# Kernel optimization log

Measured on AMD Instinct MI355X. Metric: run time of the kernel, lower is better.

## Reference

```python
import jax, jax.numpy as jnp
import numpy as np
import math

B, NB, NA, NC, D, E, H = 4, 2048, 1024, 1024, 1024, 8, 16
HD = D // H
TOP_K = 2
T_MAX = 1000.0
TAU_MIN, TAU_MAX = 0.5, 2.0
W_MIN, W_MAX = 0.1, 0.2
CAP_LO, CAP_HI = 0.5, 0.6
FLOOR = min(0.05, 0.15 / E)       # cfg.routing_floor property
ALPHA = min(FLOOR * E, 1.0)       # routing-floor interpolation weight
BIAS_COEFF = 0.01
EPS = 1e-8


def _layernorm(x, g, b, eps=1e-5):
    mu = x.mean(-1, keepdims=True)
    var = ((x - mu) ** 2).mean(-1, keepdims=True)
    return (x - mu) * jax.lax.rsqrt(var + eps) * g + b


def _forward(tokens_B, output_A, output_C, in_proj_w, in_proj_b, out_proj_w, out_proj_b,
             ln_g, ln_b, te_w1, te_b1, te_w2, te_b2,
             gate_w1, gate_b1, gate_w2, gate_b2, expert_bias, t):
    t_norm = t.astype(jnp.float32) / T_MAX                 # (B,)
    ctx_C = jax.lax.stop_gradient(output_C)                # stopgrad_C_to_B
    ctx_AC = jnp.concatenate([output_A, ctx_C], axis=1)    # (B, NA+NC, D)

    # --- cross attention (torch nn.MultiheadAttention, batch_first) ---
    wq, wk, wv = jnp.split(in_proj_w, 3, axis=0)
    bq, bk, bv = jnp.split(in_proj_b, 3)
    q = (tokens_B @ wq.T + bq).reshape(B, NB, H, HD)
    k = (ctx_AC @ wk.T + bk).reshape(B, NA + NC, H, HD)
    v = (ctx_AC @ wv.T + bv).reshape(B, NA + NC, H, HD)
    scores = jnp.einsum('bqhd,bkhd->bhqk', q, k) / math.sqrt(HD)
    attn = jax.nn.softmax(scores, axis=-1)
    ctx = jnp.einsum('bhqk,bkhd->bqhd', attn, v).reshape(B, NB, D)
    ctx_B = ctx @ out_proj_w.T + out_proj_b
    ctx_B = _layernorm(ctx_B + tokens_B, ln_g, ln_b)

    # --- sinusoidal timestep embedding + 2-layer MLP ---
    half = D // 2
    freq = jnp.exp(-math.log(10000.0) * jnp.arange(half, dtype=jnp.float32) / (half - 1))
    args = t.astype(jnp.float32)[:, None] * freq
    emb = jnp.concatenate([jnp.sin(args), jnp.cos(args)], axis=-1)   # (B, D)
    t_emb = jax.nn.silu(emb @ te_w1.T + te_b1) @ te_w2.T + te_b2     # (B, D)
    t_emb = jnp.broadcast_to(t_emb[:, None, :], (B, NB, D))

    # --- gate MLP + expert bias + temperature ---
    gate_in = jnp.concatenate([tokens_B, ctx_B, t_emb], axis=-1)     # (B, NB, 3D)
    logits = jax.nn.relu(gate_in @ gate_w1.T + gate_b1) @ gate_w2.T + gate_b2 + expert_bias
    tau = (TAU_MIN + (TAU_MAX - TAU_MIN) * t_norm)[:, None, None]
    probs = jax.nn.softmax(logits / tau, axis=-1)                    # (B, NB, E)

    # routing floor: interpolate toward uniform
    probs = (1.0 - ALPHA) * probs + ALPHA / E

    # shared expert injection: expert 0 gets scheduled weight w(t), rest renormalised
    w = (W_MIN + (W_MAX - W_MIN) * t_norm)[:, None, None]
    shared = jnp.maximum(probs[..., 0:1], w)
    others = probs[..., 1:]
    others = others / jnp.maximum(others.sum(-1, keepdims=True), EPS) * (1.0 - shared)
    probs = jnp.concatenate([shared, others], axis=-1)

    # top-k mask (keep top-k probs, zero the rest)
    vals, idx = jax.lax.top_k(probs, TOP_K)
    dispatch = (jax.nn.one_hot(idx, E, dtype=probs.dtype) * vals[..., None]).sum(-2)

    # token-level hard cap (torch.no_grad -> stop_gradient) with redistribution
    cap = (CAP_LO + (CAP_HI - CAP_LO) * t_norm)[:, None, None]
    excess = jax.nn.relu(dispatch - cap)
    capped = dispatch - excess
    headroom = jax.nn.relu(cap - capped)
    head_sum = jnp.maximum(headroom.sum(-1, keepdims=True), EPS)
    capped = capped + excess.sum(-1, keepdims=True) * (headroom / head_sum)
    dispatch = jax.lax.stop_gradient(capped)

    # batch-level utilisation penalty on specialists 1..E-1
    fair = NB / max(E - 1, 1)
    load = dispatch.sum(axis=1).mean(axis=0)                          # (E,)
    pen_excess = jax.nn.relu(load[1:] - fair * 1.5)
    bias_penalty = BIAS_COEFF * jnp.sum(pen_excess ** 2)

    combine = dispatch / (dispatch.sum(-1, keepdims=True) + EPS)
    return dispatch, combine, bias_penalty


def setup_inputs() -> dict:
    key = jax.random.key(0)
    ks = jax.random.split(key, 12)
    g = lambda k, sh: jax.random.normal(k, sh, jnp.float32) * 0.02
    return dict(
        tokens_B=jax.random.normal(ks[0], (B, NB, D), jnp.float32),
        output_A=jax.random.normal(ks[1], (B, NA, D), jnp.float32),
        output_C=jax.random.normal(ks[2], (B, NC, D), jnp.float32),
        t=jax.random.randint(ks[3], (B,), 0, 1000, jnp.int32),
        in_proj_w=g(ks[4], (3 * D, D)),
        in_proj_b=jnp.zeros((3 * D,), jnp.float32),
        out_proj_w=g(ks[5], (D, D)),
        out_proj_b=jnp.zeros((D,), jnp.float32),
        ln_g=jnp.ones((D,), jnp.float32),
        ln_b=jnp.zeros((D,), jnp.float32),
        te_w1=g(ks[6], (2 * D, D)),
        te_b1=jnp.zeros((2 * D,), jnp.float32),
        te_w2=g(ks[7], (D, 2 * D)),
        te_b2=jnp.zeros((D,), jnp.float32),
        gate_w1=g(ks[8], (D, 3 * D)),
        gate_b1=jnp.zeros((D,), jnp.float32),
        gate_w2=g(ks[9], (E, D)),
        gate_b2=jnp.zeros((E,), jnp.float32),
        expert_bias=jnp.zeros((E,), jnp.float32),
    )


def reference(tokens_B, output_A, output_C, t, in_proj_w, in_proj_b, out_proj_w, out_proj_b,
              ln_g, ln_b, te_w1, te_b1, te_w2, te_b2,
              gate_w1, gate_b1, gate_w2, gate_b2, expert_bias):
    return _forward(tokens_B, output_A, output_C, in_proj_w, in_proj_b, out_proj_w, out_proj_b,
                    ln_g, ln_b, te_w1, te_b1, te_w2, te_b2,
                    gate_w1, gate_b1, gate_w2, gate_b2, expert_bias, t)
```

## Files before the change

### kernel.cpp

```cpp
#include <hip/hip_runtime.h>
#include <math.h>


typedef __attribute__((ext_vector_type(8))) short short8;
typedef __attribute__((ext_vector_type(4))) float f32x4;
typedef unsigned short u16;
typedef unsigned int u32;

__global__ void zero_k(double* p) {
    if (threadIdx.x < 8) p[threadIdx.x] = 0.0;
}

__device__ inline u16 bf_hi(float x) {
    u32 u = __float_as_uint(x);
    u += 0x7FFFu + ((u >> 16) & 1u);
    return (u16)(u >> 16);
}
__device__ inline u16 bf_lo(float x, u16 h) {
    float hf = __uint_as_float(((u32)h) << 16);
    return bf_hi(x - hf);
}
__device__ inline u32 pack_bf(float x) {
    u32 u = __float_as_uint(x);
    u32 hi = (u + (0x7FFFu + ((u >> 16) & 1u))) >> 16;
    float hf = __uint_as_float(hi << 16);
    float d = x - hf;
    u32 u2 = __float_as_uint(d);
    u32 lo = (u2 + (0x7FFFu + ((u2 >> 16) & 1u))) >> 16;
    return (hi << 16) | lo;
}

__global__ __launch_bounds__(256)
void split_k(const float* __restrict__ in, u16* __restrict__ hi,
             u16* __restrict__ lo, int n4) {
    int i = blockIdx.x * 256 + threadIdx.x;
    if (i >= n4) return;
    float4 x = ((const float4*)in)[i];
    ushort4 h, l;
    h.x = bf_hi(x.x); l.x = bf_lo(x.x, h.x);
    h.y = bf_hi(x.y); l.y = bf_lo(x.y, h.y);
    h.z = bf_hi(x.z); l.z = bf_lo(x.z, h.z);
    h.w = bf_hi(x.w); l.w = bf_lo(x.w, h.w);
    ((ushort4*)hi)[i] = h;
    ((ushort4*)lo)[i] = l;
}

__global__ void emb_k(const int* __restrict__ t, float* __restrict__ emb) {
    int b = blockIdx.x;
    int j = threadIdx.x;
    float x1 = (float)(-9.210340371976184) * (float)j;
    float x2 = x1 / 511.0f;
    float freq = (float)exp((double)x2);
    float tf = (float)t[b];
    float arg = tf * freq;
    emb[b * 1024 + j]       = (float)sin((double)arg);
    emb[b * 1024 + 512 + j] = (float)cos((double)arg);
}

__global__ void te_fc_k(const float* __restrict__ in, const float* __restrict__ W,
                        const float* __restrict__ bias, float* __restrict__ out,
                        int K, int N, int do_silu) {
    int b = blockIdx.x;
    int wv = threadIdx.x >> 6, lane = threadIdx.x & 63;
    const float* inb = in + (size_t)b * K;
    int n0 = blockIdx.y * 16 + wv * 4;
    for (int q = 0; q < 4; q++) {
        int n = n0 + q;
        const float* wr = W + (size_t)n * K;
        float acc = 0.f;
        for (int c = lane * 4; c < K; c += 256) {
            float4 a  = *(const float4*)(inb + c);
            float4 w4 = *(const float4*)(wr + c);
            acc += a.x * w4.x + a.y * w4.y + a.z * w4.z + a.w * w4.w;
        }
#pragma unroll
        for (int off = 1; off < 64; off <<= 1) acc += __shfl_xor(acc, off, 64);
        if (lane == 0) {
            float x = acc + bias[n];
            out[(size_t)b * N + n] = do_silu ? (x / (1.0f + expf(-x))) : x;
        }
    }
}

template<bool GATE, bool RELU, int OMODE>
__global__ __launch_bounds__(256, 2)
void bfgemm_k(const u16* __restrict__ A0h, const u16* __restrict__ A0l,
              const u16* __restrict__ A1h, const u16* __restrict__ A1l,
              const u16* __restrict__ A2h, const u16* __restrict__ A2l,
              const u16* __restrict__ Wh_g, const u16* __restrict__ Wl_g,
              const float* __restrict__ bias, float* __restrict__ C,
              u16* __restrict__ Chi, u16* __restrict__ Clo, int K)
{
    __shared__ u16 Ah[128 * 32];
    __shared__ u16 Al[128 * 32];
    __shared__ u16 Wh[128 * 32];
    __shared__ u16 Wl[128 * 32];
    const int tid = threadIdx.x;
    const int row0 = blockIdx.x * 128;
    const int col0 = blockIdx.y * 128;
    const int wv = tid >> 6;
    const int lane = tid & 63;
    const int wrow = (wv & 1) * 64;
    const int wcol = (wv >> 1) * 64;
    const int l15 = lane & 15, quad = lane >> 4;

    f32x4 acc[4][4];
#pragma unroll
    for (int i = 0; i < 4; i++)
#pragma unroll
        for (int j = 0; j < 4; j++)
            acc[i][j] = (f32x4){0.f, 0.f, 0.f, 0.f};

    const int ar0 = tid >> 2, ak0 = (tid & 3) * 8;
    const int ar1 = (tid + 256) >> 2, ak1 = ((tid + 256) & 3) * 8;

    for (int kc = 0; kc < K; kc += 32) {
        const u16* pAh = A0h;
        const u16* pAl = A0l;
        int kk = kc;
        int tembseg = 0;
        if (GATE) {
            int seg = kc >> 10;
            if (seg == 1) { pAh = A1h; pAl = A1l; }
            else if (seg == 2) { pAh = A2h; pAl = A2l; tembseg = 1; }
            kk = kc & 1023;
        }
        const int astr = GATE ? 1024 : K;
        int g0 = row0 + ar0, g1 = row0 + ar1;
        if (GATE && tembseg) { g0 >>= 11; g1 >>= 11; }
        uint4 vah0 = *(const uint4*)&pAh[(size_t)g0 * astr + kk + ak0];
        uint4 vah1 = *(const uint4*)&pAh[(size_t)g1 * astr + kk + ak1];
        uint4 val0 = *(const uint4*)&pAl[(size_t)g0 * astr + kk + ak0];
        uint4 val1 = *(const uint4*)&pAl[(size_t)g1 * astr + kk + ak1];
        uint4 vwh0 = *(const uint4*)&Wh_g[(size_t)(col0 + ar0) * K + kc + ak0];
        uint4 vwh1 = *(const uint4*)&Wh_g[(size_t)(col0 + ar1) * K + kc + ak1];
        uint4 vwl0 = *(const uint4*)&Wl_g[(size_t)(col0 + ar0) * K + kc + ak0];
        uint4 vwl1 = *(const uint4*)&Wl_g[(size_t)(col0 + ar1) * K + kc + ak1];
        __syncthreads();
        *(uint4*)&Ah[ar0 * 32 + ak0] = vah0;
        *(uint4*)&Ah[ar1 * 32 + ak1] = vah1;
        *(uint4*)&Al[ar0 * 32 + ak0] = val0;
        *(uint4*)&Al[ar1 * 32 + ak1] = val1;
        *(uint4*)&Wh[ar0 * 32 + ak0] = vwh0;
        *(uint4*)&Wh[ar1 * 32 + ak1] = vwh1;
        *(uint4*)&Wl[ar0 * 32 + ak0] = vwl0;
        *(uint4*)&Wl[ar1 * 32 + ak1] = vwl1;
        __syncthreads();

        short8 a_h[4], a_l[4];
#pragma unroll
        for (int i = 0; i < 4; i++) {
            int r = (wrow + i * 16 + l15) * 32 + quad * 8;
            a_h[i] = *(const short8*)&Ah[r];
            a_l[i] = *(const short8*)&Al[r];
        }
#pragma unroll
        for (int j = 0; j < 4; j++) {
            int c = (wcol + j * 16 + l15) * 32 + quad * 8;
            short8 b_h = *(const short8*)&Wh[c];
            short8 b_l = *(const short8*)&Wl[c];
#pragma unroll
            for (int i = 0; i < 4; i++) {
                acc[i][j] = __builtin_amdgcn_mfma_f32_16x16x32_bf16(a_h[i], b_h, acc[i][j], 0, 0, 0);
                acc[i][j] = __builtin_amdgcn_mfma_f32_16x16x32_bf16(a_h[i], b_l, acc[i][j], 0, 0, 0);
                acc[i][j] = __builtin_amdgcn_mfma_f32_16x16x32_bf16(a_l[i], b_h, acc[i][j], 0, 0, 0);
            }
        }
    }

#pragma unroll
    for (int i = 0; i < 4; i++) {
#pragma unroll
        for (int j = 0; j < 4; j++) {
            int cc = col0 + wcol + j * 16 + l15;
#pragma unroll
            for (int r = 0; r < 4; r++) {
                int rr = row0 + wrow + i * 16 + quad * 4 + r;
                float v = acc[i][j][r] + ((OMODE == 3) ? bias[rr] : bias[cc]);
                if (RELU) v = fmaxf(v, 0.f);
                if (OMODE == 0) {
                    C[(size_t)rr * 1024 + cc] = v;
                } else if (OMODE == 1) {
                    u32 pk = pack_bf(v);
                    size_t a = (size_t)rr * 1024 + cc;
                    Chi[a] = (u16)(pk >> 16); Clo[a] = (u16)pk;
                } else if (OMODE == 2) {
                    int orow = ((rr >> 10) & 3) * 2048 + (rr >> 12) * 1024 + (rr & 1023);
                    u32 pk = pack_bf(v);
                    size_t a = (size_t)orow * 1024 + cc;
                    Chi[a] = (u16)(pk >> 16); Clo[a] = (u16)pk;
                } else {
                    int bb2 = (cc >> 10) & 3;
                    int key = (cc >> 12) * 1024 + (cc & 1023);
                    u32 pk = pack_bf(v);
                    size_t a = ((size_t)(bb2 * 1024 + rr)) * 2048 + key;
                    Chi[a] = (u16)(pk >> 16); Clo[a] = (u16)pk;
                }
            }
        }
    }
}

__global__ __launch_bounds__(512, 1)
void attn_k(const u16* Qh, const u16* Ql,
            const u16* __restrict__ Kh, const u16* __restrict__ Kl,
            const u16* __restrict__ Vh, const u16* __restrict__ Vl,
            u16* Oh, u16* Ol)
{
    __shared__ u32 Pu[256 * 76];
    __shared__ u16 Vsm[2][64 * 72];
    u16* Ksh = (u16*)Pu;
    u16* Ksl = Ksh + 64 * 72;

    const int tid = threadIdx.x;
    const int w = tid >> 6, lane = tid & 63;
    const int l15 = lane & 15, quad = lane >> 4;
    const int bh = blockIdx.x, b = bh >> 4, h = bh & 15;
    const int qw = blockIdx.y * 256 + w * 32;
    const int qrow0 = b * 2048 + qw;

    short8 qh_f[2][2], ql_f[2][2];
#pragma unroll
    for (int i = 0; i < 2; i++)
#pragma unroll
        for (int kc = 0; kc < 2; kc++) {
            size_t a = (size_t)(qrow0 + i * 16 + l15) * 1024 + h * 64 + kc * 32 + quad * 8;
            qh_f[i][kc] = *(const short8*)&Qh[a];
            ql_f[i][kc] = *(const short8*)&Ql[a];
        }

    const int skey = tid >> 3, sdb = (tid & 7) * 8;
    const int lds_k = skey * 72 + sdb;
    const size_t g_k = ((size_t)(b * 2048) + skey) * 1024 + h * 64 + sdb;
    const int vd = tid >> 3, vkb = (tid & 7) * 8;
    const int lds_v = vd * 72 + vkb;
    const size_t g_v = ((size_t)((b * 16 + h) * 64 + vd)) * 2048 + vkb;

    uint4 pk_h = *(const uint4*)&Kh[g_k];
    uint4 pk_l = *(const uint4*)&Kl[g_k];
    uint4 pv_h = *(const uint4*)&Vh[g_v];
    uint4 pv_l = *(const uint4*)&Vl[g_v];

    f32x4 o[2][4];
#pragma unroll
    for (int i = 0; i < 2; i++)
#pragma unroll
        for (int j = 0; j < 4; j++) o[i][j] = (f32x4){0.f, 0.f, 0.f, 0.f};
    float lsum[2][4] = {};

    for (int kt = 0; kt < 32; kt++) {
        __syncthreads();
        *(uint4*)&Ksh[lds_k] = pk_h;
        *(uint4*)&Ksl[lds_k] = pk_l;
        *(uint4*)&Vsm[0][lds_v] = pv_h;
        *(uint4*)&Vsm[1][lds_v] = pv_l;
        __syncthreads();
        if (kt < 31) {
            size_t gk2 = g_k + (size_t)(kt + 1) * 65536;
            size_t gv2 = g_v + (size_t)(kt + 1) * 64;
            pk_h = *(const uint4*)&Kh[gk2];
            pk_l = *(const uint4*)&Kl[gk2];
            pv_h = *(const uint4*)&Vh[gv2];
            pv_l = *(const uint4*)&Vl[gv2];
        }
        f32x4 s[2][4];
#pragma unroll
        for (int i = 0; i < 2; i++)
#pragma unroll
            for (int j = 0; j < 4; j++) s[i][j] = (f32x4){0.f, 0.f, 0.f, 0.f};
#pragma unroll
        for (int j = 0; j < 4; j++) {
            int ka = (j * 16 + l15) * 72 + quad * 8;
            short8 kh0 = *(const short8*)&Ksh[ka];
            short8 kh1 = *(const short8*)&Ksh[ka + 32];
            short8 kl0 = *(const short8*)&Ksl[ka];
            short8 kl1 = *(const short8*)&Ksl[ka + 32];
#pragma unroll
            for (int i = 0; i < 2; i++) {
                s[i][j] = __builtin_amdgcn_mfma_f32_16x16x32_bf16(qh_f[i][0], kh0, s[i][j], 0, 0, 0);
                s[i][j] = __builtin_amdgcn_mfma_f32_16x16x32_bf16(qh_f[i][0], kl0, s[i][j], 0, 0, 0);
                s[i][j] = __builtin_amdgcn_mfma_f32_16x16x32_bf16(ql_f[i][0], kh0, s[i][j], 0, 0, 0);
                s[i][j] = __builtin_amdgcn_mfma_f32_16x16x32_bf16(qh_f[i][1], kh1, s[i][j], 0, 0, 0);
                s[i][j] = __builtin_amdgcn_mfma_f32_16x16x32_bf16(qh_f[i][1], kl1, s[i][j], 0, 0, 0);
                s[i][j] = __builtin_amdgcn_mfma_f32_16x16x32_bf16(ql_f[i][1], kh1, s[i][j], 0, 0, 0);
            }
        }
        __syncthreads();
#pragma unroll
        for (int i = 0; i < 2; i++)
#pragma unroll
            for (int j = 0; j < 4; j++)
#pragma unroll
                for (int r = 0; r < 4; r++) {
                    float p = __expf(s[i][j][r] * 0.125f);
                    lsum[i][r] += p;
                    Pu[(w * 32 + i * 16 + quad * 4 + r) * 76 + j * 16 + l15] = pack_bf(p);
                }
#pragma unroll
        for (int kc = 0; kc < 2; kc++) {
            short8 ph[2], pl[2];
#pragma unroll
            for (int i = 0; i < 2; i++) {
                const uint4* pp = (const uint4*)&Pu[(w * 32 + i * 16 + l15) * 76 + kc * 32 + quad * 8];
                uint4 u0 = pp[0], u1 = pp[1];
                ph[i][0] = (short)(u0.x >> 16); pl[i][0] = (short)(u0.x & 0xffff);
                ph[i][1] = (short)(u0.y >> 16); pl[i][1] = (short)(u0.y & 0xffff);
                ph[i][2] = (short)(u0.z >> 16); pl[i][2] = (short)(u0.z & 0xffff);
                ph[i][3] = (short)(u0.w >> 16); pl[i][3] = (short)(u0.w & 0xffff);
                ph[i][4] = (short)(u1.x >> 16); pl[i][4] = (short)(u1.x & 0xffff);
                ph[i][5] = (short)(u1.y >> 16); pl[i][5] = (short)(u1.y & 0xffff);
                ph[i][6] = (short)(u1.z >> 16); pl[i][6] = (short)(u1.z & 0xffff);
                ph[i][7] = (short)(u1.w >> 16); pl[i][7] = (short)(u1.w & 0xffff);
            }
#pragma unroll
            for (int jd = 0; jd < 4; jd++) {
                int va = (jd * 16 + l15) * 72 + kc * 32 + quad * 8;
                short8 vvh = *(const short8*)&Vsm[0][va];
                short8 vvl = *(const short8*)&Vsm[1][va];
#pragma unroll
                for (int i = 0; i < 2; i++) {
                    o[i][jd] = __builtin_amdgcn_mfma_f32_16x16x32_bf16(ph[i], vvh, o[i][jd], 0, 0, 0);
                    o[i][jd] = __builtin_amdgcn_mfma_f32_16x16x32_bf16(ph[i], vvl, o[i][jd], 0, 0, 0);
                    o[i][jd] = __builtin_amdgcn_mfma_f32_16x16x32_bf16(pl[i], vvh, o[i][jd], 0, 0, 0);
                }
            }
        }
    }
#pragma unroll
    for (int i = 0; i < 2; i++)
#pragma unroll
        for (int r = 0; r < 4; r++) {
            float s2 = lsum[i][r];
            s2 += __shfl_xor(s2, 1, 64);
            s2 += __shfl_xor(s2, 2, 64);
            s2 += __shfl_xor(s2, 4, 64);
            s2 += __shfl_xor(s2, 8, 64);
            lsum[i][r] = s2;
        }
#pragma unroll
    for (int i = 0; i < 2; i++)
#pragma unroll
        for (int jd = 0; jd < 4; jd++)
#pragma unroll
            for (int r = 0; r < 4; r++) {
                float v = o[i][jd][r] / lsum[i][r];
                u32 pk = pack_bf(v);
                size_t a = (size_t)(qrow0 + i * 16 + quad * 4 + r) * 1024 + h * 64 + jd * 16 + l15;
                Oh[a] = (u16)(pk >> 16);
                Ol[a] = (u16)pk;
            }
}

__global__ __launch_bounds__(256)
void ln_split_k(const float* __restrict__ X, const float* __restrict__ T,
                const float* __restrict__ g, const float* __restrict__ bta,
                u16* __restrict__ chi, u16* __restrict__ clo)
{
    __shared__ float red[8];
    int r = blockIdx.x, tid = threadIdx.x;
    size_t base = (size_t)r * 1024 + tid * 4;
    float4 x  = *(const float4*)(X + base);
    float4 tk = *(const float4*)(T + base);
    x.x += tk.x; x.y += tk.y; x.z += tk.z; x.w += tk.w;
    float s = x.x + x.y + x.z + x.w;
#pragma unroll
    for (int off = 1; off < 64; off <<= 1) s += __shfl_xor(s, off, 64);
    int wv = tid >> 6;
    if ((tid & 63) == 0) red[wv] = s;
    __syncthreads();
    float mu = (red[0] + red[1] + red[2] + red[3]) * (1.0f / 1024.0f);
    float dx0 = x.x - mu, dx1 = x.y - mu, dx2 = x.z - mu, dx3 = x.w - mu;
    float ss = dx0 * dx0 + dx1 * dx1 + dx2 * dx2 + dx3 * dx3;
#pragma unroll
    for (int off = 1; off < 64; off <<= 1) ss += __shfl_xor(ss, off, 64);
    if ((tid & 63) == 0) red[4 + wv] = ss;
    __syncthreads();
    float var = (red[4] + red[5] + red[6] + red[7]) * (1.0f / 1024.0f);
    float inv = 1.0f / sqrtf(var + 1e-5f);
    float4 gg = *(const float4*)(g + tid * 4);
    float4 bb = *(const float4*)(bta + tid * 4);
    float y0 = dx0 * inv * gg.x + bb.x;
    float y1 = dx1 * inv * gg.y + bb.y;
    float y2 = dx2 * inv * gg.z + bb.z;
    float y3 = dx3 * inv * gg.w + bb.w;
    ushort4 h, l;
    h.x = bf_hi(y0); l.x = bf_lo(y0, h.x);
    h.y = bf_hi(y1); l.y = bf_lo(y1, h.y);
    h.z = bf_hi(y2); l.z = bf_lo(y2, h.z);
    h.w = bf_hi(y3); l.w = bf_lo(y3, h.w);
    *(ushort4*)&chi[base] = h;
    *(ushort4*)&clo[base] = l;
}

__global__ __launch_bounds__(256)
void logits_k(const float* __restrict__ Hd, const float* __restrict__ W2,
              const float* __restrict__ b2, const float* __restrict__ eb,
              float* __restrict__ Lg)
{
    int gw = (blockIdx.x * 256 + threadIdx.x) >> 6;
    int lane = threadIdx.x & 63;
    const float* h = Hd + (size_t)gw * 1024;
    float4 hv[4];
#pragma unroll
    for (int j = 0; j < 4; j++) hv[j] = *(const float4*)(h + j * 256 + lane * 4);
    float res[8];
#pragma unroll
    for (int e = 0; e < 8; e++) {
        const float* w = W2 + (size_t)e * 1024;
        float acc = 0.f;
#pragma unroll
        for (int j = 0; j < 4; j++) {
            float4 w4 = *(const float4*)(w + j * 256 + lane * 4);
            acc += hv[j].x * w4.x + hv[j].y * w4.y + hv[j].z * w4.z + hv[j].w * w4.w;
        }
#pragma unroll
        for (int off = 1; off < 64; off <<= 1) acc += __shfl_xor(acc, off, 64);
        res[e] = acc;
    }
    if (lane < 8) {
        float v = res[0];
#pragma unroll
        for (int e = 1; e < 8; e++) v = (lane == e) ? res[e] : v;
        Lg[(size_t)gw * 8 + lane] = v + b2[lane] + eb[lane];
    }
}

__global__ __launch_bounds__(256)
void router_k(const float* __restrict__ Lg, const int* __restrict__ t,
              float* __restrict__ outp, double* __restrict__ loadAcc)
{
    __shared__ double wred[4][8];
    int tid = threadIdx.x;
    int r = blockIdx.x * 256 + tid;
    int b = r >> 11;
    float tn  = (float)t[b] / 1000.0f;
    float tau = 0.5f + 1.5f * tn;
    float p[8];
    float mx = -INFINITY;
#pragma unroll
    for (int e = 0; e < 8; e++) { p[e] = Lg[(size_t)r * 8 + e] / tau; mx = fmaxf(mx, p[e]); }
    float sum = 0.f;
#pragma unroll
    for (int e = 0; e < 8; e++) { p[e] = expf(p[e] - mx); sum += p[e]; }
#pragma unroll
    for (int e = 0; e < 8; e++) p[e] = p[e] / sum;
#pragma unroll
    for (int e = 0; e < 8; e++) p[e] = 0.85f * p[e] + 0.01875f;
    float w = 0.1f + 0.1f * tn;
    float shared_p = fmaxf(p[0], w);
    float osum = 0.f;
#pragma unroll
    for (int e = 1; e < 8; e++) osum += p[e];
    float denom_o = fmaxf(osum, 1e-8f);
    float one_m = 1.0f - shared_p;
    p[0] = shared_p;
#pragma unroll
    for (int e = 1; e < 8; e++) p[e] = (p[e] / denom_o) * one_m;
    int i0 = 0; float v0 = p[0];
#pragma unroll
    for (int e = 1; e < 8; e++) if (p[e] > v0) { v0 = p[e]; i0 = e; }
    int i1 = -1; float v1 = -INFINITY;
#pragma unroll
    for (int e = 0; e < 8; e++) if (e != i0 && p[e] > v1) { v1 = p[e]; i1 = e; }
    float cap = 0.5f + 0.1f * tn;
    float dsp[8], capped[8], hr[8];
    float exsum = 0.f, hsum = 0.f;
#pragma unroll
    for (int e = 0; e < 8; e++) {
        float d = ((e == i0) ? v0 : 0.f) + ((e == i1) ? v1 : 0.f);
        float ex = fmaxf(d - cap, 0.f);
        float c = d - ex;
        float hh = fmaxf(cap - c, 0.f);
        capped[e] = c; hr[e] = hh;
        exsum += ex; hsum += hh;
    }
    float hden = fmaxf(hsum, 1e-8f);
    float dsum = 0.f;
#pragma unroll
    for (int e = 0; e < 8; e++) {
        float d = capped[e] + exsum * (hr[e] / hden);
        dsp[e] = d; dsum += d;
    }
    float cden = dsum + 1e-8f;
#pragma unroll
    for (int e = 0; e < 8; e++) {
        outp[(size_t)r * 8 + e] = dsp[e];
        outp[65536 + (size_t)r * 8 + e] = dsp[e] / cden;
    }
    int lane = tid & 63, wv = tid >> 6;
#pragma unroll
    for (int e = 0; e < 8; e++) {
        double s = (double)dsp[e];
#pragma unroll
        for (int off = 1; off < 64; off <<= 1) s += __shfl_xor(s, off, 64);
        if (lane == 0) wred[wv][e] = s;
    }
    __syncthreads();
    if (tid < 8) {
        double s = wred[0][tid] + wred[1][tid] + wred[2][tid] + wred[3][tid];
        atomicAdd(&loadAcc[tid], s);
    }
}

__global__ void penalty_k(const double* __restrict__ loadAcc, float* __restrict__ outp) {
    if (threadIdx.x == 0) {
        const float thr = (float)(2048.0 / 7.0 * 1.5);
        float pen = 0.f;
#pragma unroll
        for (int e = 1; e < 8; e++) {
            float load = (float)(loadAcc[e] / 4.0);
            float x = fmaxf(load - thr, 0.f);
            pen += x * x;
        }
        outp[131072] = 0.01f * pen;
    }
}

extern "C" void kernel_launch(void* const* d_in, const int* in_sizes, int n_in,
                              void* d_out, int out_size, void* d_ws, size_t ws_size,
                              hipStream_t stream)
{
    const float* tokens = (const float*)d_in[0];
    const float* outA   = (const float*)d_in[1];
    const float* outC   = (const float*)d_in[2];
    const int*   tt     = (const int*)  d_in[3];
    const float* in_w   = (const float*)d_in[4];
    const float* in_b   = (const float*)d_in[5];
    const float* op_w   = (const float*)d_in[6];
    const float* op_b   = (const float*)d_in[7];
    const float* lng    = (const float*)d_in[8];
    const float* lnb    = (const float*)d_in[9];
    const float* te_w1  = (const float*)d_in[10];
    const float* te_b1  = (const float*)d_in[11];
    const float* te_w2  = (const float*)d_in[12];
    const float* te_b2  = (const float*)d_in[13];
    const float* g_w1   = (const float*)d_in[14];
    const float* g_b1   = (const float*)d_in[15];
    const float* g_w2   = (const float*)d_in[16];
    const float* g_b2   = (const float*)d_in[17];
    const float* e_bias = (const float*)d_in[18];
    float* out = (float*)d_out;

    float* ws = (float*)d_ws;
    const size_t NM = (size_t)8192 * 1024;
    float* F0     = ws;
    float* temb   = ws + NM;
    float* embb   = temb + 4096;
    float* hte    = embb + 4096;
    float* logitsb = hte + 8192;
    double* loads = (double*)(logitsb + 65536);

    u16* U = (u16*)(loads + 16);
    u16* Tokh = U;
    u16* Tokl = Tokh + NM;
    u16* ActH = Tokl + NM;
    u16* ActL = ActH + NM;
    u16* Qh   = ActL + NM;
    u16* Ql   = Qh + NM;
    u16* Kh   = Ql + NM;
    u16* Kl   = Kh + NM;
    u16* Vth  = Kl + NM;
    u16* Vtl  = Vth + NM;
    u16* Wsh  = Vtl + NM;
    u16* Wsl  = Wsh + (size_t)3 * 1024 * 1024;
    u16* Tbh  = Wsl + (size_t)3 * 1024 * 1024;
    u16* Tbl  = Tbh + 4096;

    zero_k<<<1, 64, 0, stream>>>(loads);
    emb_k<<<4, 512, 0, stream>>>(tt, embb);
    te_fc_k<<<dim3(4, 128), 256, 0, stream>>>(embb, te_w1, te_b1, hte, 1024, 2048, 1);
    te_fc_k<<<dim3(4, 64),  256, 0, stream>>>(hte,  te_w2, te_b2, temb, 2048, 1024, 0);

    split_k<<<8192, 256, 0, stream>>>(tokens, Tokh, Tokl, 8192 * 1024 / 4);
    split_k<<<3072, 256, 0, stream>>>(in_w, Wsh, Wsl, 3 * 1024 * 1024 / 4);
    split_k<<<4096, 256, 0, stream>>>(outA, ActH, ActL, 4096 * 1024 / 4);
    split_k<<<4096, 256, 0, stream>>>(outC, ActH + (size_t)4096 * 1024,
                                      ActL + (size_t)4096 * 1024, 4096 * 1024 / 4);

    bfgemm_k<false, false, 1><<<dim3(64, 8), 256, 0, stream>>>(
        Tokh, Tokl, nullptr, nullptr, nullptr, nullptr,
        Wsh, Wsl, in_b, nullptr, Qh, Ql, 1024);
    bfgemm_k<false, false, 2><<<dim3(64, 8), 256, 0, stream>>>(
        ActH, ActL, nullptr, nullptr, nullptr, nullptr,
        Wsh + (size_t)1024 * 1024, Wsl + (size_t)1024 * 1024,
        in_b + 1024, nullptr, Kh, Kl, 1024);
    bfgemm_k<false, false, 3><<<dim3(8, 64), 256, 0, stream>>>(
        Wsh + (size_t)2048 * 1024, Wsl + (size_t)2048 * 1024,
        nullptr, nullptr, nullptr, nullptr,
        ActH, ActL, in_b + 2048, nullptr, Vth, Vtl, 1024);

    attn_k<<<dim3(64, 8), 512, 0, stream>>>(Qh, Ql, Kh, Kl, Vth, Vtl, Qh, Ql);

    split_k<<<1024, 256, 0, stream>>>(op_w, Wsh, Wsl, 1024 * 1024 / 4);
    bfgemm_k<false, false, 0><<<dim3(64, 8), 256, 0, stream>>>(
        Qh, Ql, nullptr, nullptr, nullptr, nullptr,
        Wsh, Wsl, op_b, F0, nullptr, nullptr, 1024);

    ln_split_k<<<8192, 256, 0, stream>>>(F0, tokens, lng, lnb, Kh, Kl);

    split_k<<<4, 256, 0, stream>>>(temb, Tbh, Tbl, 4096 / 4);
    split_k<<<3072, 256, 0, stream>>>(g_w1, Wsh, Wsl, 3072 * 1024 / 4);
    bfgemm_k<true, true, 0><<<dim3(64, 8), 256, 0, stream>>>(
        Tokh, Tokl, Kh, Kl, Tbh, Tbl,
        Wsh, Wsl, g_b1, F0, nullptr, nullptr, 3072);

    logits_k<<<2048, 256, 0, stream>>>(F0, g_w2, g_b2, e_bias, logitsb);
    router_k<<<32, 256, 0, stream>>>(logitsb, tt, out, loads);
    penalty_k<<<1, 64, 0, stream>>>(loads, out);
}
```

Baseline: 827.1 us.

## Swizzle attention LDS layouts, fold softmax scale into Q, use packed bf16 converts

The attention kernel's K, V and P shared-memory tiles move from padded rows to XOR-swizzled unpadded rows. This shrinks LDS use so launch bounds can request more resident blocks, while keeping bank conflicts low. The 1/sqrt(d)·log2(e) factor is folded into the Q projection epilogue, so the softmax uses exp2f with no per-element multiply. P hi/lo splitting now uses packed v_cvt_pk_bf16_f32 and byte-permute instructions instead of scalar rounding and shifts. The risks are register pressure under the higher occupancy target and subtle swizzle indexing errors.

Result: slower. 1.007 ms (+21.8%).

```diff
diff --git a/kernel.cpp b/kernel.cpp
--- a/kernel.cpp
+++ b/kernel.cpp
@@ -4,6 +4,7 @@
 
 typedef __attribute__((ext_vector_type(8))) short short8;
 typedef __attribute__((ext_vector_type(4))) float f32x4;
+typedef __attribute__((ext_vector_type(4))) unsigned int u32x4;
 typedef unsigned short u16;
 typedef unsigned int u32;
 
@@ -28,6 +29,16 @@
     u32 u2 = __float_as_uint(d);
     u32 lo = (u2 + (0x7FFFu + ((u2 >> 16) & 1u))) >> 16;
     return (hi << 16) | lo;
+}
+
+__device__ inline void pack2(float p0, float p1, u32& o0, u32& o1) {
+    u32 h01, l01;
+    asm("v_cvt_pk_bf16_f32 %0, %1, %2" : "=v"(h01) : "v"(p0), "v"(p1));
+    float d0 = p0 - __uint_as_float(h01 << 16);
+    float d1 = p1 - __uint_as_float(h01 & 0xffff0000u);
+    asm("v_cvt_pk_bf16_f32 %0, %1, %2" : "=v"(l01) : "v"(d0), "v"(d1));
+    o0 = __builtin_amdgcn_perm(h01, l01, 0x05040100u);
+    o1 = __builtin_amdgcn_perm(h01, l01, 0x07060302u);
 }
 
 __global__ __launch_bounds__(256)
@@ -89,7 +100,7 @@
               const u16* __restrict__ A2h, const u16* __restrict__ A2l,
               const u16* __restrict__ Wh_g, const u16* __restrict__ Wl_g,
               const float* __restrict__ bias, float* __restrict__ C,
-              u16* __restrict__ Chi, u16* __restrict__ Clo, int K)
+              u16* __restrict__ Chi, u16* __restrict__ Clo, int K, float scale)
 {
     __shared__ u16 Ah[128 * 32];
     __shared__ u16 Al[128 * 32];
@@ -176,7 +187,7 @@
 #pragma unroll
             for (int r = 0; r < 4; r++) {
                 int rr = row0 + wrow + i * 16 + quad * 4 + r;
-                float v = acc[i][j][r] + ((OMODE == 3) ? bias[rr] : bias[cc]);
+                float v = (acc[i][j][r] + ((OMODE == 3) ? bias[rr] : bias[cc])) * scale;
                 if (RELU) v = fmaxf(v, 0.f);
                 if (OMODE == 0) {
                     C[(size_t)rr * 1024 + cc] = v;
@@ -201,16 +212,16 @@
     }
 }
 
-__global__ __launch_bounds__(512, 1)
+__global__ __launch_bounds__(512, 4)
 void attn_k(const u16* Qh, const u16* Ql,
             const u16* __restrict__ Kh, const u16* __restrict__ Kl,
             const u16* __restrict__ Vh, const u16* __restrict__ Vl,
             u16* Oh, u16* Ol)
 {
-    __shared__ u32 Pu[256 * 76];
-    __shared__ u16 Vsm[2][64 * 72];
+    __shared__ u32 Pu[256 * 64];
+    __shared__ u16 Vsm[2][64 * 64];
     u16* Ksh = (u16*)Pu;
-    u16* Ksl = Ksh + 64 * 72;
+    u16* Ksl = Ksh + 64 * 64;
 
     const int tid = threadIdx.x;
     const int w = tid >> 6, lane = tid & 63;
@@ -229,12 +240,10 @@
             ql_f[i][kc] = *(const short8*)&Ql[a];
         }
 
-    const int skey = tid >> 3, sdb = (tid & 7) * 8;
-    const int lds_k = skey * 72 + sdb;
-    const size_t g_k = ((size_t)(b * 2048) + skey) * 1024 + h * 64 + sdb;
-    const int vd = tid >> 3, vkb = (tid & 7) * 8;
-    const int lds_v = vd * 72 + vkb;
-    const size_t g_v = ((size_t)((b * 16 + h) * 64 + vd)) * 2048 + vkb;
+    const int skey = tid >> 3, sd8 = tid & 7;
+    const int lds_kv = skey * 64 + ((sd8 ^ (skey & 7)) << 3);
+    const size_t g_k = ((size_t)(b * 2048) + skey) * 1024 + h * 64 + sd8 * 8;
+    const size_t g_v = ((size_t)((b * 16 + h) * 64 + skey)) * 2048 + sd8 * 8;
 
     uint4 pk_h = *(const uint4*)&Kh[g_k];
     uint4 pk_l = *(const uint4*)&Kl[g_k];
@@ -250,10 +259,10 @@
 
     for (int kt = 0; kt < 32; kt++) {
         __syncthreads();
-        *(uint4*)&Ksh[lds_k] = pk_h;
-        *(uint4*)&Ksl[lds_k] = pk_l;
-        *(uint4*)&Vsm[0][lds_v] = pv_h;
-        *(uint4*)&Vsm[1][lds_v] = pv_l;
+        *(uint4*)&Ksh[lds_kv] = pk_h;
+        *(uint4*)&Ksl[lds_kv] = pk_l;
+        *(uint4*)&Vsm[0][lds_kv] = pv_h;
+        *(uint4*)&Vsm[1][lds_kv] = pv_l;
         __syncthreads();
         if (kt < 31) {
             size_t gk2 = g_k + (size_t)(kt + 1) * 65536;
@@ -270,11 +279,11 @@
             for (int j = 0; j < 4; j++) s[i][j] = (f32x4){0.f, 0.f, 0.f, 0.f};
 #pragma unroll
         for (int j = 0; j < 4; j++) {
-            int ka = (j * 16 + l15) * 72 + quad * 8;
+            int ka = (j * 16 + l15) * 64 + ((quad ^ (l15 & 7)) << 3);
             short8 kh0 = *(const short8*)&Ksh[ka];
-            short8 kh1 = *(const short8*)&Ksh[ka + 32];
+            short8 kh1 = *(const short8*)&Ksh[ka ^ 32];
             short8 kl0 = *(const short8*)&Ksl[ka];
-            short8 kl1 = *(const short8*)&Ksl[ka + 32];
+            short8 kl1 = *(const short8*)&Ksl[ka ^ 32];
 #pragma unroll
             for (int i = 0; i < 2; i++) {
                 s[i][j] = __builtin_amdgcn_mfma_f32_16x16x32_bf16(qh_f[i][0], kh0, s[i][j], 0, 0, 0);
@@ -289,32 +298,46 @@
 #pragma unroll
         for (int i = 0; i < 2; i++)
 #pragma unroll
-            for (int j = 0; j < 4; j++)
-#pragma unroll
-                for (int r = 0; r < 4; r++) {
-                    float p = __expf(s[i][j][r] * 0.125f);
-                    lsum[i][r] += p;
-                    Pu[(w * 32 + i * 16 + quad * 4 + r) * 76 + j * 16 + l15] = pack_bf(p);
-                }
+            for (int j = 0; j < 4; j++) {
+                float p0 = exp2f(s[i][j][0]);
+                float p1 = exp2f(s[i][j][1]);
+                float p2 = exp2f(s[i][j][2]);
+                float p3 = exp2f(s[i][j][3]);
+                lsum[i][0] += p0; lsum[i][1] += p1;
+                lsum[i][2] += p2; lsum[i][3] += p3;
+                u32 o0, o1, o2, o3;
+                pack2(p0, p1, o0, o1);
+                pack2(p2, p3, o2, o3);
+                int rb = w * 32 + i * 16 + quad * 4;
+                int csw = (j * 16 + l15) ^ ((i * 4 + quad) << 3);
+                Pu[(rb + 0) * 64 + csw] = o0;
+                Pu[(rb + 1) * 64 + csw] = o1;
+                Pu[(rb + 2) * 64 + csw] = o2;
+                Pu[(rb + 3) * 64 + csw] = o3;
+            }
 #pragma unroll
         for (int kc = 0; kc < 2; kc++) {
             short8 ph[2], pl[2];
 #pragma unroll
             for (int i = 0; i < 2; i++) {
-                const uint4* pp = (const uint4*)&Pu[(w * 32 + i * 16 + l15) * 76 + kc * 32 + quad * 8];
+                int prow = w * 32 + i * 16 + l15;
+                int pcol = (kc * 32 + quad * 8) ^ ((i * 4 + (l15 >> 2)) << 3);
+                const uint4* pp = (const uint4*)&Pu[prow * 64 + pcol];
                 uint4 u0 = pp[0], u1 = pp[1];
-                ph[i][0] = (short)(u0.x >> 16); pl[i][0] = (short)(u0.x & 0xffff);
-                ph[i][1] = (short)(u0.y >> 16); pl[i][1] = (short)(u0.y & 0xffff);
-                ph[i][2] = (short)(u0.z >> 16); pl[i][2] = (short)(u0.z & 0xffff);
-                ph[i][3] = (short)(u0.w >> 16); pl[i][3] = (short)(u0.w & 0xffff);
-                ph[i][4] = (short)(u1.x >> 16); pl[i][4] = (short)(u1.x & 0xffff);
-                ph[i][5] = (short)(u1.y >> 16); pl[i][5] = (short)(u1.y & 0xffff);
-                ph[i][6] = (short)(u1.z >> 16); pl[i][6] = (short)(u1.z & 0xffff);
-                ph[i][7] = (short)(u1.w >> 16); pl[i][7] = (short)(u1.w & 0xffff);
+                union { short8 s; u32x4 u; } hh, ll;
+                hh.u = (u32x4){ __builtin_amdgcn_perm(u0.y, u0.x, 0x07060302u),
+                                __builtin_amdgcn_perm(u0.w, u0.z, 0x07060302u),
+                                __builtin_amdgcn_perm(u1.y, u1.x, 0x07060302u),
+                                __builtin_amdgcn_perm(u1.w, u1.z, 0x07060302u) };
+                ll.u = (u32x4){ __builtin_amdgcn_perm(u0.y, u0.x, 0x05040100u),
+                                __builtin_amdgcn_perm(u0.w, u0.z, 0x05040100u),
+                                __builtin_amdgcn_perm(u1.y, u1.x, 0x05040100u),
+                                __builtin_amdgcn_perm(u1.w, u1.z, 0x05040100u) };
+                ph[i] = hh.s; pl[i] = ll.s;
             }
 #pragma unroll
             for (int jd = 0; jd < 4; jd++) {
-                int va = (jd * 16 + l15) * 72 + kc * 32 + quad * 8;
+                int va = (jd * 16 + l15) * 64 + ((((kc << 2) + quad) ^ (l15 & 7)) << 3);
                 short8 vvh = *(const short8*)&Vsm[0][va];
                 short8 vvl = *(const short8*)&Vsm[1][va];
 #pragma unroll
@@ -579,22 +602,22 @@
 
     bfgemm_k<false, false, 1><<<dim3(64, 8), 256, 0, stream>>>(
         Tokh, Tokl, nullptr, nullptr, nullptr, nullptr,
-        Wsh, Wsl, in_b, nullptr, Qh, Ql, 1024);
+        Wsh, Wsl, in_b, nullptr, Qh, Ql, 1024, 0.18033688011112042f);
     bfgemm_k<false, false, 2><<<dim3(64, 8), 256, 0, stream>>>(
         ActH, ActL, nullptr, nullptr, nullptr, nullptr,
         Wsh + (size_t)1024 * 1024, Wsl + (size_t)1024 * 1024,
-        in_b + 1024, nullptr, Kh, Kl, 1024);
+        in_b + 1024, nullptr, Kh, Kl, 1024, 1.0f);
     bfgemm_k<false, false, 3><<<dim3(8, 64), 256, 0, stream>>>(
         Wsh + (size_t)2048 * 1024, Wsl + (size_t)2048 * 1024,
         nullptr, nullptr, nullptr, nullptr,
-        ActH, ActL, in_b + 2048, nullptr, Vth, Vtl, 1024);
+        ActH, ActL, in_b + 2048, nullptr, Vth, Vtl, 1024, 1.0f);
 
     attn_k<<<dim3(64, 8), 512, 0, stream>>>(Qh, Ql, Kh, Kl, Vth, Vtl, Qh, Ql);
 
     split_k<<<1024, 256, 0, stream>>>(op_w, Wsh, Wsl, 1024 * 1024 / 4);
     bfgemm_k<false, false, 0><<<dim3(64, 8), 256, 0, stream>>>(
         Qh, Ql, nullptr, nullptr, nullptr, nullptr,
-        Wsh, Wsl, op_b, F0, nullptr, nullptr, 1024);
+        Wsh, Wsl, op_b, F0, nullptr, nullptr, 1024, 1.0f);
 
     ln_split_k<<<8192, 256, 0, stream>>>(F0, tokens, lng, lnb, Kh, Kl);
 
@@ -602,7 +625,7 @@
     split_k<<<3072, 256, 0, stream>>>(g_w1, Wsh, Wsl, 3072 * 1024 / 4);
     bfgemm_k<true, true, 0><<<dim3(64, 8), 256, 0, stream>>>(
         Tokh, Tokl, Kh, Kl, Tbh, Tbl,
-        Wsh, Wsl, g_b1, F0, nullptr, nullptr, 3072);
+        Wsh, Wsl, g_b1, F0, nullptr, nullptr, 3072, 1.0f);
 
     logits_k<<<2048, 256, 0, stream>>>(F0, g_w2, g_b2, e_bias, logitsb);
     router_k<<<32, 256, 0, stream>>>(logitsb, tt, out, loads);
```
